# Performance work log

Measured on AMD Instinct MI355X. Metric: run time of the kernel, lower is better.

## Reference

```python
import jax, jax.numpy as jnp
import numpy as np

N_NODES = 2048
N_EDGES = 49152
R_MAX = 6.0
NUM_BASIS = 8
N_LAYERS = 4
AVG_NEIGH = 24.0
MUL_S, MUL_V = 32, 16                 # hidden irreps = 32x0e + 16x1o
N_SC_OUT = MUL_S + MUL_V              # 48 scalar channels before gate (32 scalars + 16 gates)
HID = MUL_S + 3 * MUL_V               # 80 = hidden feature dim
RAD_H = 64
# tp path weight sizes: (0e x 0e -> 0e), (1o x 1o -> 0e), (0e x 1o -> 1o), (1o x 0e -> 1o), (1o x 2e -> 1o)
N1 = MUL_S * N_SC_OUT; N2 = MUL_V * N_SC_OUT; N3 = MUL_S * MUL_V; N4 = MUL_V * MUL_V; N5 = MUL_V * MUL_V
WNUM = N1 + N2 + N3 + N4 + N5         # 3328

# orthonormal symmetric-traceless basis for real l=2 (order: xy, yz, z2, xz, x2-y2)
_s2 = 1.0 / np.sqrt(2.0); _s6 = 1.0 / np.sqrt(6.0)
_Q = np.zeros((5, 3, 3), np.float32)
_Q[0, 0, 1] = _Q[0, 1, 0] = _s2
_Q[1, 1, 2] = _Q[1, 2, 1] = _s2
_Q[2, 0, 0] = _Q[2, 1, 1] = -_s6; _Q[2, 2, 2] = 2 * _s6
_Q[3, 0, 2] = _Q[3, 2, 0] = _s2
_Q[4, 0, 0] = _s2; _Q[4, 1, 1] = -_s2
Q2 = jnp.asarray(_Q)


def _sph(d):
    # component-normalized real spherical harmonics of unit vectors d [E,3]
    x, y, z = d[:, 0], d[:, 1], d[:, 2]
    y1 = jnp.sqrt(3.0) * d
    c = jnp.sqrt(15.0)
    y2 = jnp.stack([c * x * y, c * y * z, 0.5 * jnp.sqrt(5.0) * (3 * z * z - 1.0),
                    c * x * z, 0.5 * c * (x * x - y * y)], -1)
    return y1, y2


def _bessel_cutoff(r):
    # Bessel radial basis * polynomial cutoff (p=6); r [E,1]
    n = jnp.arange(1, NUM_BASIS + 1, dtype=jnp.float32)
    rbf = jnp.sqrt(2.0 / R_MAX) * jnp.sin(n * jnp.pi * r / R_MAX) / r
    u = r / R_MAX
    f = (1.0 - 28.0 * u ** 6 + 48.0 * u ** 7 - 21.0 * u ** 8) * (u < 1.0)
    return rbf * f


def _lin(h, Ws, Wv):
    # e3nn Linear hidden -> hidden (per-irrep channel mixing, fan-in normalized)
    s = h[:, :MUL_S] @ Ws / jnp.sqrt(float(MUL_S))
    v = jnp.einsum('nui,uw->nwi', h[:, MUL_S:].reshape(-1, MUL_V, 3), Wv) / jnp.sqrt(float(MUL_V))
    return jnp.concatenate([s, v.reshape(-1, 3 * MUL_V)], -1)


def reference(x, pos, edge_index, embed_w, proj_w, lin_ws, lin_wv, sc_ws, sc_wv,
              mlp_w1, mlp_b1, mlp_w2, mlp_b2, mlp_w3, mlp_b3):
    src, dst = edge_index[0], edge_index[1]
    rel = pos[dst] - pos[src]                                   # pos_i - pos_j
    r = jnp.maximum(jnp.linalg.norm(rel, axis=-1, keepdims=True), 1e-6)
    d = rel / r
    y1, y2 = _sph(d)
    rbf = _bessel_cutoff(r)                                     # [E, 8]
    # embed: only 0e->0e path exists; 1o part starts at zero
    h = jnp.concatenate([x @ embed_w / jnp.sqrt(16.0),
                         jnp.zeros((x.shape[0], 3 * MUL_V), x.dtype)], -1)
    for l in range(N_LAYERS):
        x_res = h
        x_self = _lin(h, sc_ws[l], sc_wv[l])
        hx = _lin(h, lin_ws[l], lin_wv[l])
        # radial MLP -> per-edge tensor-product weights
        f = jax.nn.silu(rbf @ mlp_w1[l] + mlp_b1[l])
        f = jax.nn.silu(f @ mlp_w2[l] + mlp_b2[l])
        w = f @ mlp_w3[l] + mlp_b3[l]                           # [E, WNUM]
        o = 0
        w1 = w[:, o:o + N1].reshape(-1, MUL_S, N_SC_OUT); o += N1
        w2 = w[:, o:o + N2].reshape(-1, MUL_V, N_SC_OUT); o += N2
        w3 = w[:, o:o + N3].reshape(-1, MUL_S, MUL_V);    o += N3
        w4 = w[:, o:o + N4].reshape(-1, MUL_V, MUL_V);    o += N4
        w5 = w[:, o:o + N5].reshape(-1, MUL_V, MUL_V)
        s_j = hx[src, :MUL_S]
        v_j = hx[src, MUL_S:].reshape(-1, MUL_V, 3)
        # scalar outputs: (0e x 0e -> 0e) and (1o x 1o -> 0e)
        p2 = jnp.einsum('eui,ei->eu', v_j, y1) / jnp.sqrt(3.0)
        out_s = (jnp.einsum('eu,euw->ew', s_j, w1) + jnp.einsum('eu,euw->ew', p2, w2)) / jnp.sqrt(48.0)
        # vector outputs: (0e x 1o -> 1o), (1o x 0e -> 1o), (1o x 2e -> 1o)
        q3 = jnp.einsum('eu,ei->eui', s_j, y1)
        q5 = jnp.sqrt(3.0 / 5.0) * jnp.einsum('eui,em,mij->euj', v_j, y2, Q2)
        out_v = (jnp.einsum('eui,euw->ewi', q3, w3) + jnp.einsum('eui,euw->ewi', v_j, w4)
                 + jnp.einsum('eui,euw->ewi', q5, w5)) / jnp.sqrt(64.0)
        msg = jnp.concatenate([out_s, out_v.reshape(-1, 3 * MUL_V)], -1)   # [E, 96]
        agg = jax.ops.segment_sum(msg, dst, num_segments=N_NODES) / jnp.sqrt(AVG_NEIGH)
        # Gate: silu on scalars, sigmoid gates scale 1o channels
        sc = jax.nn.silu(agg[:, :MUL_S])
        g = jax.nn.sigmoid(agg[:, MUL_S:MUL_S + MUL_V])
        vec = agg[:, MUL_S + MUL_V:].reshape(-1, MUL_V, 3) * g[:, :, None]
        h = x_res + x_self + jnp.concatenate([sc, vec.reshape(-1, 3 * MUL_V)], -1)
    return h[:, :MUL_S] @ proj_w / jnp.sqrt(float(MUL_S))


def setup_inputs() -> dict:
    key = jax.random.key(0)
    ks = jax.random.split(key, 16)
    nrm = jax.random.normal
    return {
        'x': nrm(ks[0], (N_NODES, 16), jnp.float32),
        'pos': 2.0 * nrm(ks[1], (N_NODES, 3), jnp.float32),
        'edge_index': jax.random.randint(ks[2], (2, N_EDGES), 0, N_NODES),
        'embed_w': nrm(ks[3], (16, MUL_S), jnp.float32),
        'proj_w': nrm(ks[4], (MUL_S, 32), jnp.float32),
        'lin_ws': nrm(ks[5], (N_LAYERS, MUL_S, MUL_S), jnp.float32),
        'lin_wv': nrm(ks[6], (N_LAYERS, MUL_V, MUL_V), jnp.float32),
        'sc_ws': nrm(ks[7], (N_LAYERS, MUL_S, MUL_S), jnp.float32),
        'sc_wv': nrm(ks[8], (N_LAYERS, MUL_V, MUL_V), jnp.float32),
        'mlp_w1': nrm(ks[9], (N_LAYERS, NUM_BASIS, RAD_H), jnp.float32) / np.sqrt(NUM_BASIS),
        'mlp_b1': jnp.zeros((N_LAYERS, RAD_H), jnp.float32),
        'mlp_w2': nrm(ks[10], (N_LAYERS, RAD_H, RAD_H), jnp.float32) / np.sqrt(RAD_H),
        'mlp_b2': jnp.zeros((N_LAYERS, RAD_H), jnp.float32),
        'mlp_w3': nrm(ks[11], (N_LAYERS, RAD_H, WNUM), jnp.float32) / np.sqrt(RAD_H),
        'mlp_b3': jnp.zeros((N_LAYERS, WNUM), jnp.float32),
    }
```

## Files before the change

### kernel.cpp

```cpp
#include <hip/hip_runtime.h>
#include <math.h>

#define NN 2048
#define NE 49152
#define WNUM 3328

typedef __attribute__((ext_vector_type(8))) _Float16 half8;
typedef __attribute__((ext_vector_type(4))) float f32x4;

__device__ __forceinline__ float silu_f(float x){ return x / (1.0f + expf(-x)); }
__device__ __forceinline__ float sigm_f(float x){ return 1.0f / (1.0f + expf(-x)); }

__global__ void geom_kernel(const float* __restrict__ pos, const int* __restrict__ ei,
                            float* __restrict__ egeo, int* __restrict__ cnt) {
  int e = blockIdx.x * 256 + threadIdx.x;
  if (e >= NE) return;
  int s = ei[e], d = ei[NE + e];
  atomicAdd(&cnt[d], 1);
  float rx = pos[d*3+0] - pos[s*3+0];
  float ry = pos[d*3+1] - pos[s*3+1];
  float rz = pos[d*3+2] - pos[s*3+2];
  float r = sqrtf(rx*rx + ry*ry + rz*rz);
  r = fmaxf(r, 1e-6f);
  float x = rx / r, y = ry / r, z = rz / r;
  const float s3 = 1.7320508075688772f;
  const float c15 = 3.872983346207417f;
  float y2_0 = c15 * x * y;
  float y2_1 = c15 * y * z;
  float y2_2 = 1.118033988749895f * (3.0f*z*z - 1.0f);
  float y2_3 = c15 * x * z;
  float y2_4 = 1.9364916731037085f * (x*x - y*y);
  const float q2 = 0.7071067811865476f;
  const float q6 = 0.4082482904638631f;
  float* g = egeo + (size_t)e * 20;
  g[0] = s3 * x; g[1] = s3 * y; g[2] = s3 * z;
  g[3+0] = -q6*y2_2 + q2*y2_4;
  g[3+1] =  q2*y2_0;
  g[3+2] =  q2*y2_3;
  g[3+3] =  q2*y2_0;
  g[3+4] = -q6*y2_2 - q2*y2_4;
  g[3+5] =  q2*y2_1;
  g[3+6] =  q2*y2_3;
  g[3+7] =  q2*y2_1;
  g[3+8] =  2.0f*q6*y2_2;
  float u = r / 6.0f;
  float fc = 0.0f;
  if (u < 1.0f) {
    float u2=u*u, u3=u2*u, u6=u3*u3, u7=u6*u, u8=u7*u;
    fc = 1.0f - 28.0f*u6 + 48.0f*u7 - 21.0f*u8;
  }
  const float pref = 0.5773502691896258f;
  const float pi6 = 0.5235987755982988f;
  #pragma unroll
  for (int n = 1; n <= 8; n++) {
    g[12 + n - 1] = pref * sinf((float)n * pi6 * r) / r * fc;
  }
}

__global__ void scan_kernel(const int* __restrict__ cnt, int* __restrict__ offs,
                            int* __restrict__ cursor) {
  __shared__ int part[256];
  int t = threadIdx.x;
  int local[8];
  int s = 0;
  #pragma unroll
  for (int j = 0; j < 8; j++) { local[j] = s; s += cnt[t*8 + j]; }
  part[t] = s;
  __syncthreads();
  for (int off = 1; off < 256; off <<= 1) {
    int v = part[t];
    int add = (t >= off) ? part[t - off] : 0;
    __syncthreads();
    part[t] = v + add;
    __syncthreads();
  }
  int excl = (t == 0) ? 0 : part[t-1];
  #pragma unroll
  for (int j = 0; j < 8; j++) {
    int o = excl + local[j];
    offs[t*8 + j] = o;
    cursor[t*8 + j] = o;
  }
  if (t == 255) offs[2048] = part[255];
}

__global__ void scatter_kernel(const int* __restrict__ ei, int* __restrict__ cursor,
                               int* __restrict__ epos) {
  int e = blockIdx.x * 256 + threadIdx.x;
  if (e >= NE) return;
  int d = ei[NE + e];
  int p = atomicAdd(&cursor[d], 1);
  epos[e] = p;
}

__global__ void conv_w3_kernel(const float* __restrict__ w3g, _Float16* __restrict__ w3h) {
  int tid = blockIdx.x * 256 + threadIdx.x;
  if (tid >= 16 * WNUM) return;
  int n = tid % WNUM;
  int lq = tid / WNUM;
  int quad = lq & 3, l = lq >> 2;
  const float* src = w3g + (size_t)l * 64 * WNUM + n;
  int idx = n >> 4, L = n & 15;
  _Float16* dst = w3h + ((size_t)(l * 208 + idx) * 2) * 512 + (quad*16 + L) * 8;
  half8 h0, h1;
  #pragma unroll
  for (int j = 0; j < 8; j++) {
    h0[j] = (_Float16)src[(size_t)(quad*8 + j) * WNUM];
    h1[j] = (_Float16)src[(size_t)(32 + quad*8 + j) * WNUM];
  }
  *(half8*)(dst)       = h0;
  *(half8*)(dst + 512) = h1;
}

__global__ void conv_w2_kernel(const float* __restrict__ w2g, _Float16* __restrict__ w2h) {
  int tid = blockIdx.x * 256 + threadIdx.x;
  if (tid >= 16384) return;
  int j = tid & 7, lane = (tid >> 3) & 63, plane = (tid >> 9) & 1;
  int ct = (tid >> 10) & 3, l = tid >> 12;
  int q = lane >> 4, Lc = lane & 15;
  int k = plane*32 + q*8 + j;
  int n = ct*16 + Lc;
  w2h[tid] = (_Float16)w2g[(size_t)l*4096 + k*64 + n];
}

__global__ void radial_mfma_kernel(const float* __restrict__ egeo,
                                   const float* __restrict__ w1, const float* __restrict__ b1,
                                   const float* __restrict__ b2,
                                   const _Float16* __restrict__ w2h,
                                   _Float16* __restrict__ f_h) {
  __shared__ _Float16 h1s[64*72];
  const int t = threadIdx.x;
  const int l = blockIdx.x / (NE/64);
  const int e0 = (blockIdx.x % (NE/64)) * 64;
  const float* w1l = w1 + (size_t)l * 512;
  _Float16* fl = f_h + (size_t)l * NE * 64;

  {
    int e = t >> 2, jb = (t & 3) * 16;
    const float* rb = egeo + (size_t)(e0 + e) * 20 + 12;
    float r0 = rb[0], r1 = rb[1], r2 = rb[2], r3 = rb[3];
    float r4 = rb[4], r5 = rb[5], r6 = rb[6], r7 = rb[7];
    #pragma unroll
    for (int jj = 0; jj < 16; ++jj) {
      int j = jb + jj;
      float acc = b1[l*64 + j];
      acc += r0 * w1l[0*64 + j];
      acc += r1 * w1l[1*64 + j];
      acc += r2 * w1l[2*64 + j];
      acc += r3 * w1l[3*64 + j];
      acc += r4 * w1l[4*64 + j];
      acc += r5 * w1l[5*64 + j];
      acc += r6 * w1l[6*64 + j];
      acc += r7 * w1l[7*64 + j];
      h1s[e*72 + j] = (_Float16)silu_f(acc);
    }
  }
  __syncthreads();

  const int wv = t >> 6, lane = t & 63, L = lane & 15, quad = lane >> 4;
  half8 A0 = *(const half8*)&h1s[(wv*16 + L)*72 + quad*8];
  half8 A1 = *(const half8*)&h1s[(wv*16 + L)*72 + 32 + quad*8];
  #pragma unroll
  for (int ct = 0; ct < 4; ++ct) {
    const _Float16* wB = w2h + ((size_t)(l*4 + ct) * 2) * 512 + lane*8;
    half8 B0 = *(const half8*)(wB);
    half8 B1 = *(const half8*)(wB + 512);
    float bb = b2[l*64 + ct*16 + L];
    f32x4 acc = {bb, bb, bb, bb};
    acc = __builtin_amdgcn_mfma_f32_16x16x32_f16(A0, B0, acc, 0, 0, 0);
    acc = __builtin_amdgcn_mfma_f32_16x16x32_f16(A1, B1, acc, 0, 0, 0);
    #pragma unroll
    for (int r = 0; r < 4; ++r) {
      fl[(size_t)(e0 + wv*16 + quad*4 + r)*64 + ct*16 + L] = (_Float16)silu_f(acc[r]);
    }
  }
}

__global__ void embed_prep_kernel(const float* __restrict__ x, const float* __restrict__ ew,
                                  const float* __restrict__ lws0, const float* __restrict__ sws0,
                                  float* __restrict__ h, float* __restrict__ hx,
                                  float* __restrict__ xself) {
  __shared__ float hs[8][32];
  int t = threadIdx.x;
  int nl = t >> 5, c = t & 31;
  int n = blockIdx.x * 8 + nl;
  float v = 0.0f;
  #pragma unroll
  for (int j = 0; j < 16; j++) v += x[n*16 + j] * ew[j*32 + c];
  v *= 0.25f;
  hs[nl][c] = v;
  h[(size_t)n*80 + c] = v;
  for (int idx = t; idx < 8*48; idx += 256) {
    int nn = blockIdx.x * 8 + idx / 48;
    h[(size_t)nn*80 + 32 + idx % 48] = 0.0f;
  }
  __syncthreads();
  for (int idx = t; idx < 2*8*80; idx += 256) {
    int which = idx / 640, r = idx % 640;
    int nl2 = r / 80, cc = r % 80;
    int n2 = blockIdx.x * 8 + nl2;
    float o = 0.0f;
    if (cc < 32) {
      const float* W = which ? sws0 : lws0;
      #pragma unroll 8
      for (int u = 0; u < 32; u++) o += hs[nl2][u] * W[u*32 + cc];
      o *= 0.17677669529663687f;
    }
    (which ? xself : hx)[(size_t)n2*80 + cc] = o;
  }
}

__launch_bounds__(256, 2)
__global__ void edge_msg_kernel(const int* __restrict__ ei, const float* __restrict__ egeo,
                                const _Float16* __restrict__ f_h,
                                const float* __restrict__ hx,
                                const _Float16* __restrict__ w3h,
                                const float* __restrict__ b3g,
                                const int* __restrict__ epos,
                                _Float16* __restrict__ msg, int l) {
  __shared__ float smem[15616];
  __shared__ int eposS[64];
  float* sT    = smem;
  float* p2T   = smem + 2048;
  float* q3T   = smem + 3072;
  float* vT    = smem + 6144;
  float* q5T   = smem + 9216;
  float* biasL = smem + 12288;
  float* poolA = smem;
  float* poolB = smem + 3072;
  float* poolC = smem + 6144;

  const int t = threadIdx.x;
  const int e0 = blockIdx.x * 64;
  const float* b3l = b3g + (size_t)l * WNUM;

  for (int i = t; i < WNUM; i += 256) biasL[i] = b3l[i];
  if (t < 64) eposS[t] = epos[e0 + t];
  for (int idx = t; idx < 64*80; idx += 256) {
    int e = idx / 80, c = idx % 80;
    int src = ei[e0 + e];
    float val = hx[(size_t)src*80 + c];
    if (c < 32) sT[c*64 + e] = val; else vT[(c-32)*64 + e] = val;
  }
  __syncthreads();
  for (int idx = t; idx < 64*16; idx += 256) {
    int u = idx >> 6, e = idx & 63;
    const float* g = &egeo[(size_t)(e0+e)*20];
    float a = vT[(u*3)*64+e]*g[0] + vT[(u*3+1)*64+e]*g[1] + vT[(u*3+2)*64+e]*g[2];
    p2T[u*64 + e] = a * 0.5773502691896258f;
  }
  for (int idx = t; idx < 64*48; idx += 256) {
    int o = idx >> 6, e = idx & 63;
    int u = o / 3, jj = o % 3;
    const float* g = &egeo[(size_t)(e0+e)*20];
    q3T[o*64 + e] = sT[u*64 + e] * g[jj];
    float a = vT[(u*3)*64+e]*g[3+jj] + vT[(u*3+1)*64+e]*g[6+jj] + vT[(u*3+2)*64+e]*g[9+jj];
    q5T[o*64 + e] = a * 0.7745966692414834f;
  }

  const int wv = t >> 6, lane = t & 63, L = lane & 15, quad = lane >> 4;
  const int qb = quad * 4;

  half8 Ah[4][2];
  #pragma unroll
  for (int g = 0; g < 4; ++g) {
    const half8* fA = (const half8*)(f_h + (size_t)(e0 + g*16 + L)*64);
    Ah[g][0] = fA[quad];
    Ah[g][1] = fA[4 + quad];
  }
  __syncthreads();

  const _Float16* wb = w3h + (size_t)l * 208 * 1024 + lane * 8;
  half8 pb0[4], pb1[4];
  float bs[4];

#define PRIME(START)                                                          \
  { _Pragma("unroll")                                                         \
    for (int _s = 0; _s < 4; ++_s) {                                          \
      const _Float16* _wn = wb + (size_t)((START) + _s) * 1024;               \
      pb0[_s] = *(const half8*)_wn;                                           \
      pb1[_s] = *(const half8*)(_wn + 512);                                   \
      bs[_s] = biasL[((START) + _s)*16 + L];                                  \
    } }

#define GCORE(IDX, CO, OKCOND)                                                \
  f32x4 a0, a1, a2, a3;                                                       \
  { half8 _B0 = pb0[(CO)&3], _B1 = pb1[(CO)&3];                               \
    float _bb = bs[(CO)&3];                                                   \
    if (OKCOND) {                                                             \
      const _Float16* _wn = wb + (size_t)((IDX) + 4) * 1024;                  \
      pb0[(CO)&3] = *(const half8*)_wn;                                       \
      pb1[(CO)&3] = *(const half8*)(_wn + 512);                               \
      bs[(CO)&3] = biasL[((IDX) + 4)*16 + L];                                 \
    }                                                                         \
    a0 = (f32x4){_bb,_bb,_bb,_bb}; a1 = a0; a2 = a0; a3 = a0;                 \
    a0 = __builtin_amdgcn_mfma_f32_16x16x32_f16(Ah[0][0], _B0, a0, 0,0,0);    \
    a0 = __builtin_amdgcn_mfma_f32_16x16x32_f16(Ah[0][1], _B1, a0, 0,0,0);    \
    a1 = __builtin_amdgcn_mfma_f32_16x16x32_f16(Ah[1][0], _B0, a1, 0,0,0);    \
    a1 = __builtin_amdgcn_mfma_f32_16x16x32_f16(Ah[1][1], _B1, a1, 0,0,0);    \
    a2 = __builtin_amdgcn_mfma_f32_16x16x32_f16(Ah[2][0], _B0, a2, 0,0,0);    \
    a2 = __builtin_amdgcn_mfma_f32_16x16x32_f16(Ah[2][1], _B1, a2, 0,0,0);    \
    a3 = __builtin_amdgcn_mfma_f32_16x16x32_f16(Ah[3][0], _B0, a3, 0,0,0);    \
    a3 = __builtin_amdgcn_mfma_f32_16x16x32_f16(Ah[3][1], _B1, a3, 0,0,0);    \
  }

  const float S48 = 0.14433756729740645f;
  const float S64 = 0.125f;

  if (wv <= 1) {
    f32x4 ms[4][3];
    #pragma unroll
    for (int g = 0; g < 4; ++g)
      #pragma unroll
      for (int j = 0; j < 3; ++j) ms[g][j] = (f32x4){0,0,0,0};
    const int ustart = wv * 16, istart = wv * 48, iend = istart + 48;
    PRIME(istart);
    for (int u4 = 0; u4 < 16; u4 += 4) {
      #pragma unroll
      for (int uu = 0; uu < 4; ++uu) {
        const int u = u4 + uu;
        f32x4 f0 = *(const f32x4*)&sT[(ustart+u)*64 + qb];
        f32x4 f1 = *(const f32x4*)&sT[(ustart+u)*64 + 16 + qb];
        f32x4 f2 = *(const f32x4*)&sT[(ustart+u)*64 + 32 + qb];
        f32x4 f3 = *(const f32x4*)&sT[(ustart+u)*64 + 48 + qb];
        #pragma unroll
        for (int j = 0; j < 3; ++j) {
          const int CO = uu*3 + j;
          const int idx = istart + u4*3 + CO;
          GCORE(idx, CO, idx + 4 < iend);
          ms[0][j] += f0*a0; ms[1][j] += f1*a1; ms[2][j] += f2*a2; ms[3][j] += f3*a3;
        }
      }
    }
    float* pool = (wv == 0) ? poolA : poolB;
    __syncthreads();
    #pragma unroll
    for (int g = 0; g < 4; ++g)
      #pragma unroll
      for (int j = 0; j < 3; ++j)
        #pragma unroll
        for (int r = 0; r < 4; ++r)
          pool[(g*16 + qb + r)*48 + j*16 + L] = ms[g][j][r];
    __syncthreads();
  } else if (wv == 2) {
    f32x4 ms[4][3], mv[4][3];
    #pragma unroll
    for (int g = 0; g < 4; ++g)
      #pragma unroll
      for (int j = 0; j < 3; ++j) { ms[g][j] = (f32x4){0,0,0,0}; mv[g][j] = (f32x4){0,0,0,0}; }
    PRIME(96);
    for (int u4 = 0; u4 < 16; u4 += 4) {
      #pragma unroll
      for (int uu = 0; uu < 4; ++uu) {
        const int u = u4 + uu;
        f32x4 f0 = *(const f32x4*)&p2T[u*64 + qb];
        f32x4 f1 = *(const f32x4*)&p2T[u*64 + 16 + qb];
        f32x4 f2 = *(const f32x4*)&p2T[u*64 + 32 + qb];
        f32x4 f3 = *(const f32x4*)&p2T[u*64 + 48 + qb];
        #pragma unroll
        for (int j = 0; j < 3; ++j) {
          const int CO = uu*3 + j;
          const int idx = 96 + u4*3 + CO;
          GCORE(idx, CO, idx + 4 < 144);
          ms[0][j] += f0*a0; ms[1][j] += f1*a1; ms[2][j] += f2*a2; ms[3][j] += f3*a3;
        }
      }
    }
    PRIME(176);
    for (int u4 = 0; u4 < 16; u4 += 4) {
      #pragma unroll
      for (int uu = 0; uu < 4; ++uu) {
        const int u = u4 + uu;
        const int idx = 176 + u;
        GCORE(idx, uu, idx + 4 < 192);
        #pragma unroll
        for (int i = 0; i < 3; ++i) {
          mv[0][i] += *(const f32x4*)&vT[(u*3+i)*64 + qb]      * a0;
          mv[1][i] += *(const f32x4*)&vT[(u*3+i)*64 + 16 + qb] * a1;
          mv[2][i] += *(const f32x4*)&vT[(u*3+i)*64 + 32 + qb] * a2;
          mv[3][i] += *(const f32x4*)&vT[(u*3+i)*64 + 48 + qb] * a3;
        }
      }
    }
    __syncthreads();
    #pragma unroll
    for (int g = 0; g < 4; ++g)
      #pragma unroll
      for (int i = 0; i < 3; ++i)
        #pragma unroll
        for (int r = 0; r < 4; ++r)
          poolC[(g*16 + qb + r)*48 + i*16 + L] = mv[g][i][r];
    __syncthreads();
    #pragma unroll
    for (int g = 0; g < 4; ++g) {
      #pragma unroll
      for (int r = 0; r < 4; ++r) {
        const int eb = g*16 + qb + r;
        _Float16* mp = msg + (size_t)eposS[eb]*96;
        #pragma unroll
        for (int j = 0; j < 3; ++j)
          mp[j*16 + L] = (_Float16)((ms[g][j][r] + poolA[eb*48 + j*16 + L] + poolB[eb*48 + j*16 + L]) * S48);
      }
    }
  } else {
    f32x4 mv[4][3];
    #pragma unroll
    for (int g = 0; g < 4; ++g)
      #pragma unroll
      for (int i = 0; i < 3; ++i) mv[g][i] = (f32x4){0,0,0,0};
    PRIME(144);
    for (int u4 = 0; u4 < 32; u4 += 4) {
      #pragma unroll
      for (int uu = 0; uu < 4; ++uu) {
        const int u = u4 + uu;
        const int idx = 144 + u;
        GCORE(idx, uu, idx + 4 < 176);
        #pragma unroll
        for (int i = 0; i < 3; ++i) {
          mv[0][i] += *(const f32x4*)&q3T[(u*3+i)*64 + qb]      * a0;
          mv[1][i] += *(const f32x4*)&q3T[(u*3+i)*64 + 16 + qb] * a1;
          mv[2][i] += *(const f32x4*)&q3T[(u*3+i)*64 + 32 + qb] * a2;
          mv[3][i] += *(const f32x4*)&q3T[(u*3+i)*64 + 48 + qb] * a3;
        }
      }
    }
    PRIME(192);
    for (int u4 = 0; u4 < 16; u4 += 4) {
      #pragma unroll
      for (int uu = 0; uu < 4; ++uu) {
        const int u = u4 + uu;
        const int idx = 192 + u;
        GCORE(idx, uu, idx + 4 < 208);
        #pragma unroll
        for (int i = 0; i < 3; ++i) {
          mv[0][i] += *(const f32x4*)&q5T[(u*3+i)*64 + qb]      * a0;
          mv[1][i] += *(const f32x4*)&q5T[(u*3+i)*64 + 16 + qb] * a1;
          mv[2][i] += *(const f32x4*)&q5T[(u*3+i)*64 + 32 + qb] * a2;
          mv[3][i] += *(const f32x4*)&q5T[(u*3+i)*64 + 48 + qb] * a3;
        }
      }
    }
    __syncthreads();
    __syncthreads();
    #pragma unroll
    for (int g = 0; g < 4; ++g) {
      #pragma unroll
      for (int r = 0; r < 4; ++r) {
        const int eb = g*16 + qb + r;
        _Float16* mp = msg + (size_t)eposS[eb]*96;
        #pragma unroll
        for (int i = 0; i < 3; ++i)
          mp[48 + 3*L + i] = (_Float16)((mv[g][i][r] + poolC[eb*48 + i*16 + L]) * S64);
      }
    }
  }
#undef GCORE
#undef PRIME
}

__global__ void agg_fused_kernel(const _Float16* __restrict__ msg, const int* __restrict__ offs,
                                 const float* __restrict__ xself_in, float* __restrict__ h,
                                 const float* __restrict__ lwsN, const float* __restrict__ lwvN,
                                 const float* __restrict__ swsN, const float* __restrict__ swvN,
                                 float* __restrict__ hx_out, float* __restrict__ xself_out,
                                 const float* __restrict__ pw, float* __restrict__ out,
                                 int last) {
  __shared__ float sagg[4][96];
  __shared__ float hnew[4][80];
  int t = threadIdx.x;
  int nb = blockIdx.x * 4;
  for (int idx = t; idx < 4*96; idx += 256) {
    int nl = idx / 96, c = idx % 96;
    int n = nb + nl;
    int b = offs[n], e = offs[n+1];
    float acc = 0.0f, acc2 = 0.0f;
    int j = b;
    for (; j + 1 < e; j += 2) {
      acc  += (float)msg[(size_t)j*96 + c];
      acc2 += (float)msg[(size_t)(j+1)*96 + c];
    }
    if (j < e) acc += (float)msg[(size_t)j*96 + c];
    sagg[nl][c] = (acc + acc2) * 0.20412414523193154f;
  }
  __syncthreads();
  for (int idx = t; idx < 4*80; idx += 256) {
    int nl = idx / 80, c = idx % 80;
    int n = nb + nl;
    float a;
    if (c < 32) {
      a = silu_f(sagg[nl][c]);
    } else {
      int oc = c - 32, wch = oc / 3;
      a = sagg[nl][48 + oc] * sigm_f(sagg[nl][32 + wch]);
    }
    float hn = h[(size_t)n*80 + c] + xself_in[(size_t)n*80 + c] + a;
    hnew[nl][c] = hn;
    h[(size_t)n*80 + c] = hn;
  }
  __syncthreads();
  if (!last) {
    for (int idx = t; idx < 2*4*80; idx += 256) {
      int which = idx / 320, r = idx % 320;
      int nl = r / 80, c = r % 80;
      int n = nb + nl;
      const float* Ws = which ? swsN : lwsN;
      const float* Wv = which ? swvN : lwvN;
      float v = 0.0f;
      if (c < 32) {
        #pragma unroll 8
        for (int u = 0; u < 32; u++) v += hnew[nl][u] * Ws[u*32 + c];
        v *= 0.17677669529663687f;
      } else {
        int oc = c - 32, wch = oc / 3, i = oc % 3;
        #pragma unroll
        for (int u = 0; u < 16; u++) v += hnew[nl][32 + u*3 + i] * Wv[u*16 + wch];
        v *= 0.25f;
      }
      (which ? xself_out : hx_out)[(size_t)n*80 + c] = v;
    }
  } else {
    for (int idx = t; idx < 4*32; idx += 256) {
      int nl = idx / 32, c = idx % 32;
      int n = nb + nl;
      float acc = 0.0f;
      #pragma unroll 8
      for (int u = 0; u < 32; u++) acc += hnew[nl][u] * pw[u*32 + c];
      out[(size_t)n*32 + c] = acc * 0.17677669529663687f;
    }
  }
}

extern "C" void kernel_launch(void* const* d_in, const int* in_sizes, int n_in,
                              void* d_out, int out_size, void* d_ws, size_t ws_size,
                              hipStream_t stream) {
  const float* x       = (const float*)d_in[0];
  const float* pos     = (const float*)d_in[1];
  const int*   ei      = (const int*)  d_in[2];
  const float* embed_w = (const float*)d_in[3];
  const float* proj_w  = (const float*)d_in[4];
  const float* lin_ws  = (const float*)d_in[5];
  const float* lin_wv  = (const float*)d_in[6];
  const float* sc_ws   = (const float*)d_in[7];
  const float* sc_wv   = (const float*)d_in[8];
  const float* mlp_w1  = (const float*)d_in[9];
  const float* mlp_b1  = (const float*)d_in[10];
  const float* mlp_w2  = (const float*)d_in[11];
  const float* mlp_b2  = (const float*)d_in[12];
  const float* mlp_w3  = (const float*)d_in[13];
  const float* mlp_b3  = (const float*)d_in[14];
  float* out = (float*)d_out;

  float* ws    = (float*)d_ws;
  float* egeo  = ws;
  float* h     = egeo  + (size_t)NE*20;
  float* hx    = h     + (size_t)NN*80;
  float* xself = hx    + (size_t)NN*80;
  _Float16* msg = (_Float16*)(xself + (size_t)NN*80);
  _Float16* f_h = msg + (size_t)NE*96;
  _Float16* w3h = f_h + (size_t)4*NE*64;
  _Float16* w2h = w3h + (size_t)4*208*1024;
  int* cnt    = (int*)(w2h + 16384);
  int* offs   = cnt + NN;
  int* cursor = offs + NN + 1;
  int* epos   = cursor + NN;

  hipMemsetAsync(cnt, 0, NN*sizeof(int), stream);
  geom_kernel<<<(NE + 255)/256, 256, 0, stream>>>(pos, ei, egeo, cnt);
  scan_kernel<<<1, 256, 0, stream>>>(cnt, offs, cursor);
  scatter_kernel<<<NE/256, 256, 0, stream>>>(ei, cursor, epos);
  conv_w3_kernel<<<(16*WNUM + 255)/256, 256, 0, stream>>>(mlp_w3, w3h);
  conv_w2_kernel<<<64, 256, 0, stream>>>(mlp_w2, w2h);
  radial_mfma_kernel<<<4*(NE/64), 256, 0, stream>>>(egeo, mlp_w1, mlp_b1, mlp_b2, w2h, f_h);
  embed_prep_kernel<<<NN/8, 256, 0, stream>>>(x, embed_w, lin_ws, sc_ws, h, hx, xself);

  for (int l = 0; l < 4; l++) {
    edge_msg_kernel<<<NE/64, 256, 0, stream>>>(ei, egeo, f_h + (size_t)l*NE*64, hx,
                                               w3h, mlp_b3, epos, msg, l);
    int last = (l == 3);
    agg_fused_kernel<<<NN/4, 256, 0, stream>>>(
        msg, offs, xself, h,
        lin_ws + (size_t)(l+1 < 4 ? l+1 : 0) * 1024,
        lin_wv + (size_t)(l+1 < 4 ? l+1 : 0) * 256,
        sc_ws  + (size_t)(l+1 < 4 ? l+1 : 0) * 1024,
        sc_wv  + (size_t)(l+1 < 4 ? l+1 : 0) * 256,
        hx, xself, proj_w, out, last);
  }
}
```

Baseline: 443.6 us.

## Fuse prologue kernels into one launch and store hx in half precision

Merges the scatter, w3 conversion, radial MLP and embedding kernels into a single block-range-dispatched prologue kernel, cutting four launches to one and letting independent work overlap. It also stores the per-node hx features as fp16 instead of fp32, halving the bytes of the gathered source features read in each edge_msg layer. The fp16 storage adds rounding error to messages. The __syncthreads in the radial and embed branches is only reached by blocks of that branch, so it is safe.

```diff
diff --git a/kernel.cpp b/kernel.cpp
--- a/kernel.cpp
+++ b/kernel.cpp
@@ -84,34 +84,6 @@
   if (t == 255) offs[2048] = part[255];
 }
 
-__global__ void scatter_kernel(const int* __restrict__ ei, int* __restrict__ cursor,
-                               int* __restrict__ epos) {
-  int e = blockIdx.x * 256 + threadIdx.x;
-  if (e >= NE) return;
-  int d = ei[NE + e];
-  int p = atomicAdd(&cursor[d], 1);
-  epos[e] = p;
-}
-
-__global__ void conv_w3_kernel(const float* __restrict__ w3g, _Float16* __restrict__ w3h) {
-  int tid = blockIdx.x * 256 + threadIdx.x;
-  if (tid >= 16 * WNUM) return;
-  int n = tid % WNUM;
-  int lq = tid / WNUM;
-  int quad = lq & 3, l = lq >> 2;
-  const float* src = w3g + (size_t)l * 64 * WNUM + n;
-  int idx = n >> 4, L = n & 15;
-  _Float16* dst = w3h + ((size_t)(l * 208 + idx) * 2) * 512 + (quad*16 + L) * 8;
-  half8 h0, h1;
-  #pragma unroll
-  for (int j = 0; j < 8; j++) {
-    h0[j] = (_Float16)src[(size_t)(quad*8 + j) * WNUM];
-    h1[j] = (_Float16)src[(size_t)(32 + quad*8 + j) * WNUM];
-  }
-  *(half8*)(dst)       = h0;
-  *(half8*)(dst + 512) = h1;
-}
-
 __global__ void conv_w2_kernel(const float* __restrict__ w2g, _Float16* __restrict__ w2h) {
   int tid = blockIdx.x * 256 + threadIdx.x;
   if (tid >= 16384) return;
@@ -123,97 +95,128 @@
   w2h[tid] = (_Float16)w2g[(size_t)l*4096 + k*64 + n];
 }
 
-__global__ void radial_mfma_kernel(const float* __restrict__ egeo,
-                                   const float* __restrict__ w1, const float* __restrict__ b1,
-                                   const float* __restrict__ b2,
-                                   const _Float16* __restrict__ w2h,
-                                   _Float16* __restrict__ f_h) {
-  __shared__ _Float16 h1s[64*72];
+#define PB_SCAT  192
+#define PB_W3    208
+#define PB_RAD   3072
+#define PB_EMB   256
+__global__ void prologue_fused_kernel(
+    const int* __restrict__ ei, int* __restrict__ cursor, int* __restrict__ epos,
+    const float* __restrict__ w3g, _Float16* __restrict__ w3h,
+    const _Float16* __restrict__ w2h,
+    const float* __restrict__ egeo,
+    const float* __restrict__ w1, const float* __restrict__ b1,
+    const float* __restrict__ b2, _Float16* __restrict__ f_h,
+    const float* __restrict__ x, const float* __restrict__ ew,
+    const float* __restrict__ lws0, const float* __restrict__ sws0,
+    float* __restrict__ h, _Float16* __restrict__ hx, float* __restrict__ xself) {
+  __shared__ float smem[2304];
+  const int blk = blockIdx.x;
   const int t = threadIdx.x;
-  const int l = blockIdx.x / (NE/64);
-  const int e0 = (blockIdx.x % (NE/64)) * 64;
-  const float* w1l = w1 + (size_t)l * 512;
-  _Float16* fl = f_h + (size_t)l * NE * 64;
-
-  {
-    int e = t >> 2, jb = (t & 3) * 16;
-    const float* rb = egeo + (size_t)(e0 + e) * 20 + 12;
-    float r0 = rb[0], r1 = rb[1], r2 = rb[2], r3 = rb[3];
-    float r4 = rb[4], r5 = rb[5], r6 = rb[6], r7 = rb[7];
-    #pragma unroll
-    for (int jj = 0; jj < 16; ++jj) {
-      int j = jb + jj;
-      float acc = b1[l*64 + j];
-      acc += r0 * w1l[0*64 + j];
-      acc += r1 * w1l[1*64 + j];
-      acc += r2 * w1l[2*64 + j];
-      acc += r3 * w1l[3*64 + j];
-      acc += r4 * w1l[4*64 + j];
-      acc += r5 * w1l[5*64 + j];
-      acc += r6 * w1l[6*64 + j];
-      acc += r7 * w1l[7*64 + j];
-      h1s[e*72 + j] = (_Float16)silu_f(acc);
-    }
-  }
-  __syncthreads();
-
-  const int wv = t >> 6, lane = t & 63, L = lane & 15, quad = lane >> 4;
-  half8 A0 = *(const half8*)&h1s[(wv*16 + L)*72 + quad*8];
-  half8 A1 = *(const half8*)&h1s[(wv*16 + L)*72 + 32 + quad*8];
-  #pragma unroll
-  for (int ct = 0; ct < 4; ++ct) {
-    const _Float16* wB = w2h + ((size_t)(l*4 + ct) * 2) * 512 + lane*8;
-    half8 B0 = *(const half8*)(wB);
-    half8 B1 = *(const half8*)(wB + 512);
-    float bb = b2[l*64 + ct*16 + L];
-    f32x4 acc = {bb, bb, bb, bb};
-    acc = __builtin_amdgcn_mfma_f32_16x16x32_f16(A0, B0, acc, 0, 0, 0);
-    acc = __builtin_amdgcn_mfma_f32_16x16x32_f16(A1, B1, acc, 0, 0, 0);
-    #pragma unroll
-    for (int r = 0; r < 4; ++r) {
-      fl[(size_t)(e0 + wv*16 + quad*4 + r)*64 + ct*16 + L] = (_Float16)silu_f(acc[r]);
-    }
-  }
-}
-
-__global__ void embed_prep_kernel(const float* __restrict__ x, const float* __restrict__ ew,
-                                  const float* __restrict__ lws0, const float* __restrict__ sws0,
-                                  float* __restrict__ h, float* __restrict__ hx,
-                                  float* __restrict__ xself) {
-  __shared__ float hs[8][32];
-  int t = threadIdx.x;
-  int nl = t >> 5, c = t & 31;
-  int n = blockIdx.x * 8 + nl;
-  float v = 0.0f;
-  #pragma unroll
-  for (int j = 0; j < 16; j++) v += x[n*16 + j] * ew[j*32 + c];
-  v *= 0.25f;
-  hs[nl][c] = v;
-  h[(size_t)n*80 + c] = v;
-  for (int idx = t; idx < 8*48; idx += 256) {
-    int nn = blockIdx.x * 8 + idx / 48;
-    h[(size_t)nn*80 + 32 + idx % 48] = 0.0f;
-  }
-  __syncthreads();
-  for (int idx = t; idx < 2*8*80; idx += 256) {
-    int which = idx / 640, r = idx % 640;
-    int nl2 = r / 80, cc = r % 80;
-    int n2 = blockIdx.x * 8 + nl2;
-    float o = 0.0f;
-    if (cc < 32) {
-      const float* W = which ? sws0 : lws0;
-      #pragma unroll 8
-      for (int u = 0; u < 32; u++) o += hs[nl2][u] * W[u*32 + cc];
-      o *= 0.17677669529663687f;
-    }
-    (which ? xself : hx)[(size_t)n2*80 + cc] = o;
+
+  if (blk < PB_SCAT) {
+    int e = blk * 256 + t;
+    int d = ei[NE + e];
+    int p = atomicAdd(&cursor[d], 1);
+    epos[e] = p;
+  } else if (blk < PB_SCAT + PB_W3) {
+    int tid = (blk - PB_SCAT) * 256 + t;
+    if (tid >= 16 * WNUM) return;
+    int n = tid % WNUM;
+    int lq = tid / WNUM;
+    int quad = lq & 3, l = lq >> 2;
+    const float* src = w3g + (size_t)l * 64 * WNUM + n;
+    int idx = n >> 4, L = n & 15;
+    _Float16* dst = w3h + ((size_t)(l * 208 + idx) * 2) * 512 + (quad*16 + L) * 8;
+    half8 h0, h1;
+    #pragma unroll
+    for (int j = 0; j < 8; j++) {
+      h0[j] = (_Float16)src[(size_t)(quad*8 + j) * WNUM];
+      h1[j] = (_Float16)src[(size_t)(32 + quad*8 + j) * WNUM];
+    }
+    *(half8*)(dst)       = h0;
+    *(half8*)(dst + 512) = h1;
+  } else if (blk < PB_SCAT + PB_W3 + PB_RAD) {
+    _Float16* h1s = (_Float16*)smem;
+    int rb = blk - PB_SCAT - PB_W3;
+    const int l = rb / (NE/64);
+    const int e0 = (rb % (NE/64)) * 64;
+    const float* w1l = w1 + (size_t)l * 512;
+    _Float16* fl = f_h + (size_t)l * NE * 64;
+    {
+      int e = t >> 2, jb = (t & 3) * 16;
+      const float* rbp = egeo + (size_t)(e0 + e) * 20 + 12;
+      float r0 = rbp[0], r1 = rbp[1], r2 = rbp[2], r3 = rbp[3];
+      float r4 = rbp[4], r5 = rbp[5], r6 = rbp[6], r7 = rbp[7];
+      #pragma unroll
+      for (int jj = 0; jj < 16; ++jj) {
+        int j = jb + jj;
+        float acc = b1[l*64 + j];
+        acc += r0 * w1l[0*64 + j];
+        acc += r1 * w1l[1*64 + j];
+        acc += r2 * w1l[2*64 + j];
+        acc += r3 * w1l[3*64 + j];
+        acc += r4 * w1l[4*64 + j];
+        acc += r5 * w1l[5*64 + j];
+        acc += r6 * w1l[6*64 + j];
+        acc += r7 * w1l[7*64 + j];
+        h1s[e*72 + j] = (_Float16)silu_f(acc);
+      }
+    }
+    __syncthreads();
+    const int wv = t >> 6, lane = t & 63, L = lane & 15, quad = lane >> 4;
+    half8 A0 = *(const half8*)&h1s[(wv*16 + L)*72 + quad*8];
+    half8 A1 = *(const half8*)&h1s[(wv*16 + L)*72 + 32 + quad*8];
+    #pragma unroll
+    for (int ct = 0; ct < 4; ++ct) {
+      const _Float16* wB = w2h + ((size_t)(l*4 + ct) * 2) * 512 + lane*8;
+      half8 B0 = *(const half8*)(wB);
+      half8 B1 = *(const half8*)(wB + 512);
+      float bb = b2[l*64 + ct*16 + L];
+      f32x4 acc = {bb, bb, bb, bb};
+      acc = __builtin_amdgcn_mfma_f32_16x16x32_f16(A0, B0, acc, 0, 0, 0);
+      acc = __builtin_amdgcn_mfma_f32_16x16x32_f16(A1, B1, acc, 0, 0, 0);
+      #pragma unroll
+      for (int r = 0; r < 4; ++r) {
+        fl[(size_t)(e0 + wv*16 + quad*4 + r)*64 + ct*16 + L] = (_Float16)silu_f(acc[r]);
+      }
+    }
+  } else {
+    float* hs = smem;
+    int rb = blk - PB_SCAT - PB_W3 - PB_RAD;
+    int nl = t >> 5, c = t & 31;
+    int n = rb * 8 + nl;
+    float v = 0.0f;
+    #pragma unroll
+    for (int j = 0; j < 16; j++) v += x[n*16 + j] * ew[j*32 + c];
+    v *= 0.25f;
+    hs[nl*32 + c] = v;
+    h[(size_t)n*80 + c] = v;
+    for (int idx = t; idx < 8*48; idx += 256) {
+      int nn = rb * 8 + idx / 48;
+      h[(size_t)nn*80 + 32 + idx % 48] = 0.0f;
+    }
+    __syncthreads();
+    for (int idx = t; idx < 2*8*80; idx += 256) {
+      int which = idx / 640, r = idx % 640;
+      int nl2 = r / 80, cc = r % 80;
+      int n2 = rb * 8 + nl2;
+      float o = 0.0f;
+      if (cc < 32) {
+        const float* W = which ? sws0 : lws0;
+        #pragma unroll 8
+        for (int u = 0; u < 32; u++) o += hs[nl2*32 + u] * W[u*32 + cc];
+        o *= 0.17677669529663687f;
+      }
+      if (which) xself[(size_t)n2*80 + cc] = o;
+      else       hx[(size_t)n2*80 + cc] = (_Float16)o;
+    }
   }
 }
 
 __launch_bounds__(256, 2)
 __global__ void edge_msg_kernel(const int* __restrict__ ei, const float* __restrict__ egeo,
                                 const _Float16* __restrict__ f_h,
-                                const float* __restrict__ hx,
+                                const _Float16* __restrict__ hx,
                                 const _Float16* __restrict__ w3h,
                                 const float* __restrict__ b3g,
                                 const int* __restrict__ epos,
@@ -239,7 +242,7 @@
   for (int idx = t; idx < 64*80; idx += 256) {
     int e = idx / 80, c = idx % 80;
     int src = ei[e0 + e];
-    float val = hx[(size_t)src*80 + c];
+    float val = (float)hx[(size_t)src*80 + c];
     if (c < 32) sT[c*64 + e] = val; else vT[(c-32)*64 + e] = val;
   }
   __syncthreads();
@@ -462,7 +465,7 @@
                                  const float* __restrict__ xself_in, float* __restrict__ h,
                                  const float* __restrict__ lwsN, const float* __restrict__ lwvN,
                                  const float* __restrict__ swsN, const float* __restrict__ swvN,
-                                 float* __restrict__ hx_out, float* __restrict__ xself_out,
+                                 _Float16* __restrict__ hx_out, float* __restrict__ xself_out,
                                  const float* __restrict__ pw, float* __restrict__ out,
                                  int last) {
   __shared__ float sagg[4][96];
@@ -516,7 +519,8 @@
         for (int u = 0; u < 16; u++) v += hnew[nl][32 + u*3 + i] * Wv[u*16 + wch];
         v *= 0.25f;
       }
-      (which ? xself_out : hx_out)[(size_t)n*80 + c] = v;
+      if (which) xself_out[(size_t)n*80 + c] = v;
+      else       hx_out[(size_t)n*80 + c] = (_Float16)v;
     }
   } else {
     for (int idx = t; idx < 4*32; idx += 256) {
@@ -553,9 +557,9 @@
   float* ws    = (float*)d_ws;
   float* egeo  = ws;
   float* h     = egeo  + (size_t)NE*20;
-  float* hx    = h     + (size_t)NN*80;
-  float* xself = hx    + (size_t)NN*80;
-  _Float16* msg = (_Float16*)(xself + (size_t)NN*80);
+  float* xself = h     + (size_t)NN*80;
+  _Float16* hx  = (_Float16*)(xself + (size_t)NN*80);
+  _Float16* msg = hx + (size_t)NN*80;
   _Float16* f_h = msg + (size_t)NE*96;
   _Float16* w3h = f_h + (size_t)4*NE*64;
   _Float16* w2h = w3h + (size_t)4*208*1024;
@@ -567,11 +571,10 @@
   hipMemsetAsync(cnt, 0, NN*sizeof(int), stream);
   geom_kernel<<<(NE + 255)/256, 256, 0, stream>>>(pos, ei, egeo, cnt);
   scan_kernel<<<1, 256, 0, stream>>>(cnt, offs, cursor);
-  scatter_kernel<<<NE/256, 256, 0, stream>>>(ei, cursor, epos);
-  conv_w3_kernel<<<(16*WNUM + 255)/256, 256, 0, stream>>>(mlp_w3, w3h);
   conv_w2_kernel<<<64, 256, 0, stream>>>(mlp_w2, w2h);
-  radial_mfma_kernel<<<4*(NE/64), 256, 0, stream>>>(egeo, mlp_w1, mlp_b1, mlp_b2, w2h, f_h);
-  embed_prep_kernel<<<NN/8, 256, 0, stream>>>(x, embed_w, lin_ws, sc_ws, h, hx, xself);
+  prologue_fused_kernel<<<PB_SCAT + PB_W3 + PB_RAD + PB_EMB, 256, 0, stream>>>(
+      ei, cursor, epos, mlp_w3, w3h, w2h, egeo,
+      mlp_w1, mlp_b1, mlp_b2, f_h, x, embed_w, lin_ws, sc_ws, h, hx, xself);
 
   for (int l = 0; l < 4; l++) {
     edge_msg_kernel<<<NE/64, 256, 0, stream>>>(ei, egeo, f_h + (size_t)l*NE*64, hx,
```

After: 429.9 us. 3.1% less time.
